# Kernel optimization log

Hardware: AMD Instinct MI355X
Metric: run time of the kernel (lower is better)

The kernel has to match this reference:

```python
import jax, jax.numpy as jnp
import numpy as np

MODEL_DIM = 768
EMB_DIM = 768
NUM_HEADS = 12
HEAD_DIM = MODEL_DIM // NUM_HEADS  # 64
B, S = 4, 1024
LN_EPS = 1e-12


def setup_inputs() -> dict:
    key = jax.random.key(0)
    ks = jax.random.split(key, 12)
    s_in = 1.0 / np.sqrt(EMB_DIM)
    s_dm = 1.0 / np.sqrt(MODEL_DIM)
    return {
        "x": jax.random.normal(ks[0], (B, S, EMB_DIM), dtype=jnp.float32),
        # stacked per-head projection weights, [H, E, Dh] (in, out layout)
        "Wq": jax.random.normal(ks[1], (NUM_HEADS, EMB_DIM, HEAD_DIM), dtype=jnp.float32) * s_in,
        "bq": jax.random.normal(ks[2], (NUM_HEADS, HEAD_DIM), dtype=jnp.float32) * 0.02,
        "Wk": jax.random.normal(ks[3], (NUM_HEADS, EMB_DIM, HEAD_DIM), dtype=jnp.float32) * s_in,
        "bk": jax.random.normal(ks[4], (NUM_HEADS, HEAD_DIM), dtype=jnp.float32) * 0.02,
        "Wv": jax.random.normal(ks[5], (NUM_HEADS, EMB_DIM, HEAD_DIM), dtype=jnp.float32) * s_in,
        "bv": jax.random.normal(ks[6], (NUM_HEADS, HEAD_DIM), dtype=jnp.float32) * 0.02,
        # output dense [Dm, Dm] (in, out) + bias
        "Wd": jax.random.normal(ks[7], (MODEL_DIM, MODEL_DIM), dtype=jnp.float32) * s_dm,
        "bd": jax.random.normal(ks[8], (MODEL_DIM,), dtype=jnp.float32) * 0.02,
        # LayerNorm affine params
        "gamma": jnp.ones((MODEL_DIM,), dtype=jnp.float32),
        "beta": jnp.zeros((MODEL_DIM,), dtype=jnp.float32),
    }


def reference(x, Wq, bq, Wk, bk, Wv, bv, Wd, bd, gamma, beta):
    # Batched per-head projections: [B,S,E] x [H,E,Dh] -> [B,H,S,Dh]
    Q = jnp.einsum("bse,hed->bhsd", x, Wq) + bq[None, :, None, :]
    K = jnp.einsum("bse,hed->bhsd", x, Wk) + bk[None, :, None, :]
    V = jnp.einsum("bse,hed->bhsd", x, Wv) + bv[None, :, None, :]

    scale = 1.0 / jnp.sqrt(jnp.asarray(HEAD_DIM, dtype=Q.dtype))
    scores = jnp.einsum("bhsd,bhtd->bhst", Q, K) * scale  # [B,H,S,S]
    weights = jax.nn.softmax(scores, axis=-1)
    ctx = jnp.einsum("bhst,bhtd->bhsd", weights, V)  # [B,H,S,Dh]

    # concat per-head outputs along last dim (head order): [B,S,H*Dh]
    outputs = jnp.transpose(ctx, (0, 2, 1, 3)).reshape(B, S, NUM_HEADS * HEAD_DIM)
    # concat per-head attention weights along last dim: [B,S,H*S]
    weights_cat = jnp.transpose(weights, (0, 2, 1, 3)).reshape(B, S, NUM_HEADS * S)

    # BertSelfOutput: dense -> LayerNorm (dropout = identity in eval)
    y = jnp.einsum("bsi,io->bso", outputs, Wd) + bd
    mu = jnp.mean(y, axis=-1, keepdims=True)
    var = jnp.mean(jnp.square(y - mu), axis=-1, keepdims=True)
    y = (y - mu) * jax.lax.rsqrt(var + LN_EPS) * gamma + beta
    return weights_cat, y
```

## Files before the change

kernel.cpp:

```cpp
#include <hip/hip_runtime.h>

typedef __bf16 bf16x8 __attribute__((ext_vector_type(8)));
typedef float  f32x4  __attribute__((ext_vector_type(4)));
typedef unsigned short u16x8 __attribute__((ext_vector_type(8)));
typedef unsigned short u16x4 __attribute__((ext_vector_type(4)));

__device__ __forceinline__ unsigned short f2bf(float f) {
  union { float f; unsigned u; } v; v.f = f;
  unsigned r = v.u + 0x7fffu + ((v.u >> 16) & 1u);
  return (unsigned short)(r >> 16);
}

__device__ __forceinline__ float bf2f(unsigned short b) {
  union { unsigned u; float f; } v; v.u = (unsigned)b << 16;
  return v.f;
}

__device__ __forceinline__ void gload16(const unsigned short* g, unsigned short* l) {
  __builtin_amdgcn_global_load_lds(
      (const __attribute__((address_space(1))) unsigned int*)g,
      (__attribute__((address_space(3))) unsigned int*)l,
      16, 0, 0);
}

__device__ __forceinline__ void nt_store4(float* p, f32x4 v) {
  __builtin_nontemporal_store(v, (f32x4*)p);
}

#define WOFF 50331648

__global__ __launch_bounds__(256) void prep(
    const float* __restrict__ x, const float* __restrict__ Wq, const float* __restrict__ Wk,
    const float* __restrict__ Wv, const float* __restrict__ Wd,
    unsigned short* __restrict__ xb, unsigned short* __restrict__ wb, unsigned short* __restrict__ wdb)
{
  __shared__ float t[32][33];
  const int bid = blockIdx.x, tid = threadIdx.x;
  if (bid < 1536) {
    int i = (bid * 256 + tid) * 8;
    f32x4 v0 = *(const f32x4*)&x[i];
    f32x4 v1 = *(const f32x4*)&x[i + 4];
    u16x8 o;
    for (int j = 0; j < 4; j++) { o[j] = f2bf(v0[j]); o[j + 4] = f2bf(v1[j]); }
    *(u16x8*)&xb[i] = o;
    return;
  }
  const int tx = tid & 31, ty = tid >> 5;
  if (bid < 3264) {
    int q = bid - 1536;
    int bx = q & 1; q >>= 1;
    int by = q % 24, z = q / 24;
    int m = z / 12;
    const float* in = (m == 0 ? Wq : m == 1 ? Wk : Wv) + (long)(z % 12) * 49152;
    unsigned short* ob = wb + (long)z * 49152;
    int c = bx * 32 + tx, r0 = by * 32;
    for (int i = ty; i < 32; i += 8) t[i][tx] = in[(long)(r0 + i) * 64 + c];
    __syncthreads();
    int c0 = bx * 32;
    for (int i = ty; i < 32; i += 8) ob[(long)(c0 + i) * 768 + r0 + tx] = f2bf(t[tx][i]);
    return;
  }
  {
    int q = bid - 3264;
    int bx = q % 24, by = q / 24;
    int c = bx * 32 + tx, r0 = by * 32;
    for (int i = ty; i < 32; i += 8) t[i][tx] = Wd[(long)(r0 + i) * 768 + c];
    __syncthreads();
    int c0 = bx * 32;
    for (int i = ty; i < 32; i += 8) wdb[(long)(c0 + i) * 768 + r0 + tx] = f2bf(t[tx][i]);
  }
}

__global__ __launch_bounds__(256) void qkv_gemm(
    const unsigned short* __restrict__ xb, const unsigned short* __restrict__ wb,
    const float* __restrict__ bq, const float* __restrict__ bk, const float* __restrict__ bv,
    unsigned short* __restrict__ Qb, unsigned short* __restrict__ Kb, unsigned short* __restrict__ Vt)
{
  __shared__ unsigned short As[2][4096];
  __shared__ unsigned short Bs[2][4096];
  const int tid = threadIdx.x;
  const int bid = blockIdx.x;
  const int swz = (bid & 7) * 72 + (bid >> 3);
  const int bn = (swz % 18) * 128, bm = (swz / 18) * 128;
  const int w = tid >> 6, l = tid & 63;
  const int wr = w >> 1, wc = w & 1;
  const int lr = l & 15, lg = l >> 4;

  f32x4 acc[4][4];
  for (int i = 0; i < 4; i++) for (int j = 0; j < 4; j++) acc[i][j] = {0.f, 0.f, 0.f, 0.f};

  const unsigned short* ga = xb + (long)(bm + (tid >> 2)) * 768 + (tid & 3) * 8;
  const unsigned short* gb = wb + (long)(bn + (tid >> 2)) * 768 + (tid & 3) * 8;
  const int lofs = w << 9;

  gload16(ga,            &As[0][lofs]);
  gload16(ga + 64 * 768, &As[0][lofs + 2048]);
  gload16(gb,            &Bs[0][lofs]);
  gload16(gb + 64 * 768, &Bs[0][lofs + 2048]);
  __syncthreads();

  int cur = 0;
  for (int t = 0; t < 24; t++) {
    if (t < 23) {
      int k0 = (t + 1) * 32;
      gload16(ga + k0,            &As[cur ^ 1][lofs]);
      gload16(ga + k0 + 64 * 768, &As[cur ^ 1][lofs + 2048]);
      gload16(gb + k0,            &Bs[cur ^ 1][lofs]);
      gload16(gb + k0 + 64 * 768, &Bs[cur ^ 1][lofs + 2048]);
    }
    bf16x8 af[4], bfv[4];
    for (int i = 0; i < 4; i++) af[i]  = *(const bf16x8*)&As[cur][(wr * 64 + i * 16 + lr) * 32 + lg * 8];
    for (int j = 0; j < 4; j++) bfv[j] = *(const bf16x8*)&Bs[cur][(wc * 64 + j * 16 + lr) * 32 + lg * 8];
    for (int i = 0; i < 4; i++)
      for (int j = 0; j < 4; j++)
        acc[i][j] = __builtin_amdgcn_mfma_f32_16x16x32_bf16(af[i], bfv[j], acc[i][j], 0, 0, 0);
    __syncthreads();
    cur ^= 1;
  }

  for (int i = 0; i < 4; i++) for (int j = 0; j < 4; j++) {
    int col = bn + wc * 64 + j * 16 + lr;
    int m = col / 768, rc = col % 768;
    int h = rc >> 6, d = rc & 63;
    const float* bias = (m == 0) ? bq : (m == 1) ? bk : bv;
    float bb = bias[rc];
    for (int r = 0; r < 4; r++) {
      int row = bm + wr * 64 + i * 16 + lg * 4 + r;
      int b = row >> 10, s = row & 1023;
      float v = acc[i][j][r] + bb;
      if (m == 0)      Qb[((b * 12 + h) << 16) + (s << 6) + d] = f2bf(v * 0.125f);
      else if (m == 1) Kb[((b * 12 + h) << 16) + (s << 6) + d] = f2bf(v);
      else             Vt[((b * 12 + h) << 16) + (d << 10) + s] = f2bf(v);
    }
  }
}

__global__ __launch_bounds__(512) void attn_kernel(
    const unsigned short* __restrict__ Qb, const unsigned short* __restrict__ Kb,
    const unsigned short* __restrict__ Vt,
    float* __restrict__ wout, unsigned short* __restrict__ ctx)
{
  extern __shared__ char smem[];
  unsigned short* E  = (unsigned short*)smem;
  unsigned short* Qs = (unsigned short*)(smem + 66048);
  float* sred = (float*)(smem + 70656);
  float* sfin = (float*)(smem + 71680);

  const int bid = blockIdx.x;
  const int swz = (bid & 7) * 192 + (bid >> 3);
  const int bh = swz >> 5;
  const int q0 = (swz & 31) * 32;
  const int b = bh / 12, h = bh % 12;
  const int tid = threadIdx.x;
  const int w = tid >> 6, l = tid & 63, lr = l & 15, lg = l >> 4;
  const unsigned short* Qg = Qb + (bh << 16);
  const unsigned short* Kg = Kb + (bh << 16);
  const unsigned short* Vg = Vt + (bh << 16);

  if (tid < 256) {
    int row = tid >> 3, c = (tid & 7) * 8;
    *(u16x8*)&Qs[row * 72 + c] = *(const u16x8*)&Qg[(q0 + row) * 64 + c];
  }
  __syncthreads();

  bf16x8 qa[2][2];
  for (int ri = 0; ri < 2; ri++) {
    qa[ri][0] = *(const bf16x8*)&Qs[(ri * 16 + lr) * 72 + lg * 8];
    qa[ri][1] = *(const bf16x8*)&Qs[(ri * 16 + lr) * 72 + 32 + lg * 8];
  }
  f32x4 sc[2][8];
#pragma unroll
  for (int cf = 0; cf < 8; cf++) {
    int colb = w * 128 + cf * 16;
    bf16x8 kb0 = *(const bf16x8*)&Kg[(colb + lr) * 64 + lg * 8];
    bf16x8 kb1 = *(const bf16x8*)&Kg[(colb + lr) * 64 + 32 + lg * 8];
#pragma unroll
    for (int ri = 0; ri < 2; ri++) {
      f32x4 a = {0.f, 0.f, 0.f, 0.f};
      a = __builtin_amdgcn_mfma_f32_16x16x32_bf16(qa[ri][0], kb0, a, 0, 0, 0);
      a = __builtin_amdgcn_mfma_f32_16x16x32_bf16(qa[ri][1], kb1, a, 0, 0, 0);
      sc[ri][cf] = a;
    }
  }

  float sm[2][4] = {{0.f, 0.f, 0.f, 0.f}, {0.f, 0.f, 0.f, 0.f}};
#pragma unroll
  for (int cf = 0; cf < 8; cf++)
#pragma unroll
    for (int ri = 0; ri < 2; ri++)
#pragma unroll
      for (int r = 0; r < 4; r++) {
        float e = __expf(sc[ri][cf][r]);
        sm[ri][r] += e;
        E[(ri * 16 + lg * 4 + r) * 1032 + w * 128 + cf * 16 + lr] = f2bf(e);
      }
#pragma unroll
  for (int ri = 0; ri < 2; ri++)
#pragma unroll
    for (int r = 0; r < 4; r++) {
      float s = sm[ri][r];
      for (int o = 8; o >= 1; o >>= 1) s += __shfl_xor(s, o, 16);
      if (lr == 0) sred[w * 32 + ri * 16 + lg * 4 + r] = s;
    }
  __syncthreads();
  if (tid < 32) {
    float s = 0.f;
    for (int ww = 0; ww < 8; ww++) s += sred[ww * 32 + tid];
    sfin[tid] = 1.f / s;
  }
  __syncthreads();

  {
    float* wbase = wout + (long)(b * 1024 + q0) * 12288 + h * 1024;
#pragma unroll
    for (int it = 0; it < 16; it++) {
      int vidx = it * 512 + tid;
      int row = vidx >> 8, c4 = (vidx & 255) * 4;
      float rs = sfin[row];
      u16x4 ev = *(const u16x4*)&E[row * 1032 + c4];
      f32x4 o;
      for (int t = 0; t < 4; t++) o[t] = bf2f(ev[t]) * rs;
      nt_store4(&wbase[(long)row * 12288 + c4], o);
    }
  }

  {
    int ri = w >> 2, cf = w & 3;
    f32x4 acc = {0.f, 0.f, 0.f, 0.f};
#pragma unroll
    for (int ks = 0; ks < 32; ks++) {
      int kk = ks * 32;
      bf16x8 pa = *(const bf16x8*)&E[(ri * 16 + lr) * 1032 + kk + lg * 8];
      bf16x8 vb = *(const bf16x8*)&Vg[(cf * 16 + lr) * 1024 + kk + lg * 8];
      acc = __builtin_amdgcn_mfma_f32_16x16x32_bf16(pa, vb, acc, 0, 0, 0);
    }
    for (int r = 0; r < 4; r++) {
      int row = ri * 16 + lg * 4 + r;
      Qs[row * 72 + cf * 16 + lr] = f2bf(acc[r] * sfin[row]);
    }
  }
  __syncthreads();
  if (tid < 256) {
    int row = tid >> 3, c = (tid & 7) * 8;
    *(u16x8*)&ctx[(long)(b * 1024 + q0 + row) * 768 + h * 64 + c] = *(const u16x8*)&Qs[row * 72 + c];
  }
}

__global__ __launch_bounds__(256) void dense_gemm(
    const unsigned short* __restrict__ ctx, const unsigned short* __restrict__ wdb,
    const float* __restrict__ bd, float* __restrict__ y)
{
  __shared__ unsigned short As[2][2048];
  __shared__ unsigned short Bs[2][4096];
  const int tid = threadIdx.x;
  const int bid = blockIdx.x;
  const int swz = (bid & 7) * 48 + (bid >> 3);
  const int bn = (swz % 6) * 128, bm = (swz / 6) * 64;
  const int w = tid >> 6, l = tid & 63;
  const int wr = w >> 1, wc = w & 1;
  const int lr = l & 15, lg = l >> 4;

  f32x4 acc[2][4];
  for (int i = 0; i < 2; i++) for (int j = 0; j < 4; j++) acc[i][j] = {0.f, 0.f, 0.f, 0.f};

  const unsigned short* ga = ctx + (long)(bm + (tid >> 2)) * 768 + (tid & 3) * 8;
  const unsigned short* gb = wdb + (long)(bn + (tid >> 2)) * 768 + (tid & 3) * 8;
  const int lofs = w << 9;

  gload16(ga,            &As[0][lofs]);
  gload16(gb,            &Bs[0][lofs]);
  gload16(gb + 64 * 768, &Bs[0][lofs + 2048]);
  __syncthreads();

  int cur = 0;
  for (int t = 0; t < 24; t++) {
    if (t < 23) {
      int k0 = (t + 1) * 32;
      gload16(ga + k0,            &As[cur ^ 1][lofs]);
      gload16(gb + k0,            &Bs[cur ^ 1][lofs]);
      gload16(gb + k0 + 64 * 768, &Bs[cur ^ 1][lofs + 2048]);
    }
    bf16x8 af[2], bfv[4];
    for (int i = 0; i < 2; i++) af[i]  = *(const bf16x8*)&As[cur][(wr * 32 + i * 16 + lr) * 32 + lg * 8];
    for (int j = 0; j < 4; j++) bfv[j] = *(const bf16x8*)&Bs[cur][(wc * 64 + j * 16 + lr) * 32 + lg * 8];
    for (int i = 0; i < 2; i++)
      for (int j = 0; j < 4; j++)
        acc[i][j] = __builtin_amdgcn_mfma_f32_16x16x32_bf16(af[i], bfv[j], acc[i][j], 0, 0, 0);
    __syncthreads();
    cur ^= 1;
  }

  for (int i = 0; i < 2; i++) for (int j = 0; j < 4; j++) {
    int col = bn + wc * 64 + j * 16 + lr;
    float bb = bd[col];
    for (int r = 0; r < 4; r++) {
      int row = bm + wr * 32 + i * 16 + lg * 4 + r;
      y[(long)row * 768 + col] = acc[i][j][r] + bb;
    }
  }
}

__global__ __launch_bounds__(256) void ln_kernel(
    const float* __restrict__ y,
    const float* __restrict__ gamma, const float* __restrict__ beta,
    float* __restrict__ out)
{
  int w = threadIdx.x >> 6, l = threadIdx.x & 63;
  long row = blockIdx.x * 4 + w;
  const float* yr = y + row * 768;
  f32x4 v[3];
  float s = 0.f, ss = 0.f;
  for (int j = 0; j < 3; j++) {
    int c = j * 256 + l * 4;
    f32x4 t = *(const f32x4*)&yr[c];
    for (int q = 0; q < 4; q++) { s += t[q]; ss += t[q] * t[q]; }
    v[j] = t;
  }
  for (int o = 32; o >= 1; o >>= 1) { s += __shfl_xor(s, o); ss += __shfl_xor(ss, o); }
  float mu = s * (1.f / 768.f);
  float var = ss * (1.f / 768.f) - mu * mu;
  float rs = rsqrtf(var + 1e-12f);
  float* orow = out + row * 768;
  for (int j = 0; j < 3; j++) {
    int c = j * 256 + l * 4;
    f32x4 g = *(const f32x4*)&gamma[c];
    f32x4 be = *(const f32x4*)&beta[c];
    f32x4 o;
    for (int q = 0; q < 4; q++) o[q] = (v[j][q] - mu) * rs * g[q] + be[q];
    nt_store4(&orow[c], o);
  }
}

extern "C" void kernel_launch(void* const* d_in, const int* in_sizes, int n_in,
                              void* d_out, int out_size, void* d_ws, size_t ws_size,
                              hipStream_t stream) {
  const float* x     = (const float*)d_in[0];
  const float* Wq    = (const float*)d_in[1];
  const float* bq    = (const float*)d_in[2];
  const float* Wk    = (const float*)d_in[3];
  const float* bk    = (const float*)d_in[4];
  const float* Wv    = (const float*)d_in[5];
  const float* bv    = (const float*)d_in[6];
  const float* Wd    = (const float*)d_in[7];
  const float* bd    = (const float*)d_in[8];
  const float* gamma = (const float*)d_in[9];
  const float* beta  = (const float*)d_in[10];
  float* out = (float*)d_out;

  char* ws = (char*)d_ws;
  unsigned short* xb  = (unsigned short*)(ws);
  unsigned short* wb  = (unsigned short*)(ws + 6291456);
  unsigned short* wdb = (unsigned short*)(ws + 9830400);
  unsigned short* Qb  = (unsigned short*)(ws + 11010048);
  unsigned short* Kb  = (unsigned short*)(ws + 17301504);
  unsigned short* Vt  = (unsigned short*)(ws + 23592960);
  unsigned short* ctx = (unsigned short*)(ws + 29884416);
  float*          yws = (float*)(ws + 11010048);

  prep<<<3840, 256, 0, stream>>>(x, Wq, Wk, Wv, Wd, xb, wb, wdb);
  qkv_gemm<<<576, 256, 0, stream>>>(xb, wb, bq, bk, bv, Qb, Kb, Vt);
  attn_kernel<<<1536, 512, 71808, stream>>>(Qb, Kb, Vt, out, ctx);
  dense_gemm<<<384, 256, 0, stream>>>(ctx, wdb, bd, yws);
  ln_kernel<<<1024, 256, 0, stream>>>(yws, gamma, beta, out + WOFF);
}
```

Baseline: 152.1 us.

## Halve attention query tile to 16 rows, swizzle E buffer, split-K PV reduction

The attention kernel now processes 16 query rows per block instead of 32 and launches twice as many blocks. Shared memory drops from about 72KB to about 44KB, which allows more blocks per CU. The exp buffer uses an XOR-swizzled layout in place of row padding to avoid LDS bank conflicts. The PV product is split across two K halves and summed through a shared fp32 buffer. Weight output stores switch from nontemporal to normal stores, and each block now reloads K and V for half as many queries, which doubles K/V traffic.

After: 169.6 us. +11.5%, slower.

```diff
diff --git a/kernel.cpp b/kernel.cpp
--- a/kernel.cpp
+++ b/kernel.cpp
@@ -28,6 +28,10 @@
 }
 
 #define WOFF 50331648
+
+__device__ __forceinline__ int eidx(int row, int col) {
+  return row * 1024 + ((((col >> 3) ^ (row & 7)) << 3) | (col & 7));
+}
 
 __global__ __launch_bounds__(256) void prep(
     const float* __restrict__ x, const float* __restrict__ Wq, const float* __restrict__ Wk,
@@ -49,10 +53,10 @@
   if (bid < 3264) {
     int q = bid - 1536;
     int bx = q & 1; q >>= 1;
-    int by = q % 24, z = q / 24;
-    int m = z / 12;
-    const float* in = (m == 0 ? Wq : m == 1 ? Wk : Wv) + (long)(z % 12) * 49152;
-    unsigned short* ob = wb + (long)z * 49152;
+    int by = q % 24, zz = q / 24;
+    int m = zz / 12;
+    const float* in = (m == 0 ? Wq : m == 1 ? Wk : Wv) + (long)(zz % 12) * 49152;
+    unsigned short* ob = wb + (long)zz * 49152;
     int c = bx * 32 + tx, r0 = by * 32;
     for (int i = ty; i < 32; i += 8) t[i][tx] = in[(long)(r0 + i) * 64 + c];
     __syncthreads();
@@ -85,13 +89,13 @@
   const int w = tid >> 6, l = tid & 63;
   const int wr = w >> 1, wc = w & 1;
   const int lr = l & 15, lg = l >> 4;
+  const int lofs = w << 9;
 
   f32x4 acc[4][4];
   for (int i = 0; i < 4; i++) for (int j = 0; j < 4; j++) acc[i][j] = {0.f, 0.f, 0.f, 0.f};
 
   const unsigned short* ga = xb + (long)(bm + (tid >> 2)) * 768 + (tid & 3) * 8;
   const unsigned short* gb = wb + (long)(bn + (tid >> 2)) * 768 + (tid & 3) * 8;
-  const int lofs = w << 9;
 
   gload16(ga,            &As[0][lofs]);
   gload16(ga + 64 * 768, &As[0][lofs + 2048]);
@@ -142,14 +146,15 @@
 {
   extern __shared__ char smem[];
   unsigned short* E  = (unsigned short*)smem;
-  unsigned short* Qs = (unsigned short*)(smem + 66048);
-  float* sred = (float*)(smem + 70656);
-  float* sfin = (float*)(smem + 71680);
+  unsigned short* Qs = (unsigned short*)(smem + 32768);
+  float* pacc = (float*)(smem + 35072);
+  float* sred = (float*)(smem + 43264);
+  float* sfin = (float*)(smem + 43776);
 
   const int bid = blockIdx.x;
-  const int swz = (bid & 7) * 192 + (bid >> 3);
-  const int bh = swz >> 5;
-  const int q0 = (swz & 31) * 32;
+  const int swz = (bid & 7) * 384 + (bid >> 3);
+  const int bh = swz >> 6;
+  const int q0 = (swz & 63) * 16;
   const int b = bh / 12, h = bh % 12;
   const int tid = threadIdx.x;
   const int w = tid >> 6, l = tid & 63, lr = l & 15, lg = l >> 4;
@@ -157,55 +162,45 @@
   const unsigned short* Kg = Kb + (bh << 16);
   const unsigned short* Vg = Vt + (bh << 16);
 
-  if (tid < 256) {
+  if (tid < 128) {
     int row = tid >> 3, c = (tid & 7) * 8;
     *(u16x8*)&Qs[row * 72 + c] = *(const u16x8*)&Qg[(q0 + row) * 64 + c];
   }
   __syncthreads();
 
-  bf16x8 qa[2][2];
-  for (int ri = 0; ri < 2; ri++) {
-    qa[ri][0] = *(const bf16x8*)&Qs[(ri * 16 + lr) * 72 + lg * 8];
-    qa[ri][1] = *(const bf16x8*)&Qs[(ri * 16 + lr) * 72 + 32 + lg * 8];
-  }
-  f32x4 sc[2][8];
+  bf16x8 qa0 = *(const bf16x8*)&Qs[lr * 72 + lg * 8];
+  bf16x8 qa1 = *(const bf16x8*)&Qs[lr * 72 + 32 + lg * 8];
+  f32x4 sc[8];
 #pragma unroll
   for (int cf = 0; cf < 8; cf++) {
     int colb = w * 128 + cf * 16;
     bf16x8 kb0 = *(const bf16x8*)&Kg[(colb + lr) * 64 + lg * 8];
     bf16x8 kb1 = *(const bf16x8*)&Kg[(colb + lr) * 64 + 32 + lg * 8];
-#pragma unroll
-    for (int ri = 0; ri < 2; ri++) {
-      f32x4 a = {0.f, 0.f, 0.f, 0.f};
-      a = __builtin_amdgcn_mfma_f32_16x16x32_bf16(qa[ri][0], kb0, a, 0, 0, 0);
-      a = __builtin_amdgcn_mfma_f32_16x16x32_bf16(qa[ri][1], kb1, a, 0, 0, 0);
-      sc[ri][cf] = a;
-    }
-  }
-
-  float sm[2][4] = {{0.f, 0.f, 0.f, 0.f}, {0.f, 0.f, 0.f, 0.f}};
+    f32x4 a = {0.f, 0.f, 0.f, 0.f};
+    a = __builtin_amdgcn_mfma_f32_16x16x32_bf16(qa0, kb0, a, 0, 0, 0);
+    a = __builtin_amdgcn_mfma_f32_16x16x32_bf16(qa1, kb1, a, 0, 0, 0);
+    sc[cf] = a;
+  }
+
+  float sm[4] = {0.f, 0.f, 0.f, 0.f};
 #pragma unroll
   for (int cf = 0; cf < 8; cf++)
 #pragma unroll
-    for (int ri = 0; ri < 2; ri++)
-#pragma unroll
-      for (int r = 0; r < 4; r++) {
-        float e = __expf(sc[ri][cf][r]);
-        sm[ri][r] += e;
-        E[(ri * 16 + lg * 4 + r) * 1032 + w * 128 + cf * 16 + lr] = f2bf(e);
-      }
-#pragma unroll
-  for (int ri = 0; ri < 2; ri++)
-#pragma unroll
     for (int r = 0; r < 4; r++) {
-      float s = sm[ri][r];
-      for (int o = 8; o >= 1; o >>= 1) s += __shfl_xor(s, o, 16);
-      if (lr == 0) sred[w * 32 + ri * 16 + lg * 4 + r] = s;
-    }
-  __syncthreads();
-  if (tid < 32) {
+      float e = __expf(sc[cf][r]);
+      sm[r] += e;
+      E[eidx(lg * 4 + r, w * 128 + cf * 16 + lr)] = f2bf(e);
+    }
+#pragma unroll
+  for (int r = 0; r < 4; r++) {
+    float s = sm[r];
+    for (int o = 8; o >= 1; o >>= 1) s += __shfl_xor(s, o, 16);
+    if (lr == 0) sred[w * 16 + lg * 4 + r] = s;
+  }
+  __syncthreads();
+  if (tid < 16) {
     float s = 0.f;
-    for (int ww = 0; ww < 8; ww++) s += sred[ww * 32 + tid];
+    for (int ww = 0; ww < 8; ww++) s += sred[ww * 16 + tid];
     sfin[tid] = 1.f / s;
   }
   __syncthreads();
@@ -213,36 +208,37 @@
   {
     float* wbase = wout + (long)(b * 1024 + q0) * 12288 + h * 1024;
 #pragma unroll
-    for (int it = 0; it < 16; it++) {
+    for (int it = 0; it < 8; it++) {
       int vidx = it * 512 + tid;
       int row = vidx >> 8, c4 = (vidx & 255) * 4;
       float rs = sfin[row];
-      u16x4 ev = *(const u16x4*)&E[row * 1032 + c4];
+      u16x4 ev = *(const u16x4*)&E[eidx(row, c4)];
       f32x4 o;
       for (int t = 0; t < 4; t++) o[t] = bf2f(ev[t]) * rs;
-      nt_store4(&wbase[(long)row * 12288 + c4], o);
+      *(f32x4*)&wbase[(long)row * 12288 + c4] = o;
     }
   }
 
   {
-    int ri = w >> 2, cf = w & 3;
+    int kh = w >> 2, cf = w & 3;
     f32x4 acc = {0.f, 0.f, 0.f, 0.f};
 #pragma unroll
-    for (int ks = 0; ks < 32; ks++) {
-      int kk = ks * 32;
-      bf16x8 pa = *(const bf16x8*)&E[(ri * 16 + lr) * 1032 + kk + lg * 8];
+    for (int ks = 0; ks < 16; ks++) {
+      int kk = kh * 512 + ks * 32;
+      bf16x8 pa = *(const bf16x8*)&E[eidx(lr, kk + lg * 8)];
       bf16x8 vb = *(const bf16x8*)&Vg[(cf * 16 + lr) * 1024 + kk + lg * 8];
       acc = __builtin_amdgcn_mfma_f32_16x16x32_bf16(pa, vb, acc, 0, 0, 0);
     }
-    for (int r = 0; r < 4; r++) {
-      int row = ri * 16 + lg * 4 + r;
-      Qs[row * 72 + cf * 16 + lr] = f2bf(acc[r] * sfin[row]);
-    }
-  }
-  __syncthreads();
-  if (tid < 256) {
-    int row = tid >> 3, c = (tid & 7) * 8;
-    *(u16x8*)&ctx[(long)(b * 1024 + q0 + row) * 768 + h * 64 + c] = *(const u16x8*)&Qs[row * 72 + c];
+    for (int r = 0; r < 4; r++)
+      pacc[(kh * 16 + lg * 4 + r) * 64 + cf * 16 + lr] = acc[r];
+  }
+  __syncthreads();
+#pragma unroll
+  for (int it = 0; it < 2; it++) {
+    int e = it * 512 + tid;
+    int row = e >> 6, d = e & 63;
+    float v = (pacc[row * 64 + d] + pacc[(16 + row) * 64 + d]) * sfin[row];
+    ctx[(long)(b * 1024 + q0 + row) * 768 + h * 64 + d] = f2bf(v);
   }
 }
 
@@ -259,13 +255,13 @@
   const int w = tid >> 6, l = tid & 63;
   const int wr = w >> 1, wc = w & 1;
   const int lr = l & 15, lg = l >> 4;
+  const int lofs = w << 9;
 
   f32x4 acc[2][4];
   for (int i = 0; i < 2; i++) for (int j = 0; j < 4; j++) acc[i][j] = {0.f, 0.f, 0.f, 0.f};
 
   const unsigned short* ga = ctx + (long)(bm + (tid >> 2)) * 768 + (tid & 3) * 8;
   const unsigned short* gb = wdb + (long)(bn + (tid >> 2)) * 768 + (tid & 3) * 8;
-  const int lofs = w << 9;
 
   gload16(ga,            &As[0][lofs]);
   gload16(gb,            &Bs[0][lofs]);
@@ -359,7 +355,7 @@
 
   prep<<<3840, 256, 0, stream>>>(x, Wq, Wk, Wv, Wd, xb, wb, wdb);
   qkv_gemm<<<576, 256, 0, stream>>>(xb, wb, bq, bk, bv, Qb, Kb, Vt);
-  attn_kernel<<<1536, 512, 71808, stream>>>(Qb, Kb, Vt, out, ctx);
+  attn_kernel<<<3072, 512, 43840, stream>>>(Qb, Kb, Vt, out, ctx);
   dense_gemm<<<384, 256, 0, stream>>>(ctx, wdb, bd, yws);
   ln_kernel<<<1024, 256, 0, stream>>>(yws, gamma, beta, out + WOFF);
 }
```
